# Kernel optimization log

Measured on AMD Instinct MI355X. Metric: run time of the kernel, lower is better.

## Reference

```python
import jax, jax.numpy as jnp
import numpy as np

DEPTH = 10
LAMDA = 1e-3
EPS = 1e-7


def setup_inputs() -> dict:
    key = jax.random.key(0)
    k1, k2, k3, k4 = jax.random.split(key, 4)
    B, D, O = 16384, 512, 256
    N = 2 ** DEPTH - 1        # inner nodes
    L = 2 ** DEPTH            # leaves
    data = jax.random.normal(k1, (B, D), jnp.float32)
    # small scale on W keeps sigmoid away from saturation (like nn.Linear init)
    W = jax.random.normal(k2, (N, D + 1), jnp.float32) * 0.02
    beta = jax.random.normal(k3, (N,), jnp.float32)
    param = jax.random.normal(k4, (L, O), jnp.float32)
    return {"data": data, "W": W, "beta": beta, "param": param}


def reference(data, W, beta, param):
    B = data.shape[0]
    L = param.shape[0]
    # _data_augment_: prepend constant 1 as bias feature -> [B, D+1]
    x = jnp.concatenate([jnp.ones((B, 1), data.dtype), data], axis=1)
    # inner_nodes: sigmoid(beta * linear(x)) -> [B, N]
    p = jax.nn.sigmoid(beta * (x @ W.T))
    # per-node (go-left, go-right) probabilities -> [B, N, 2]
    path_prob = jnp.stack([p, 1.0 - p], axis=2)

    mu = jnp.ones((B, 1), data.dtype)          # path prob of root
    penalty = jnp.asarray(0.0, data.dtype)
    begin = 0
    for layer in range(DEPTH):                  # fixed small loop over depth
        n = 2 ** layer
        pp = path_prob[:, begin:begin + n, :].reshape(B, 2 * n)  # [B, 2n]
        mu_rep = jnp.repeat(mu, 2, axis=1)                        # [B, 2n]
        # vectorized form of the per-node penalty loop
        alpha = jnp.sum(pp * mu_rep, axis=0) / (jnp.sum(mu_rep, axis=0) + EPS)
        alpha = jnp.clip(alpha, EPS, 1.0 - EPS)
        coeff = LAMDA * (2.0 ** (-layer))
        penalty = penalty - coeff * 0.5 * jnp.sum(jnp.log(alpha) + jnp.log(1.0 - alpha))
        mu = mu_rep * pp
        begin += n

    # mu: [B, leaf_num]; leaf_nodes: mu @ softmax(param)
    dist = jax.nn.softmax(param, axis=1)       # [L, O]
    output = mu @ dist                          # [B, O]
    # greatest_path_probability: hard argmax leaf (one-hot @ dist == gather)
    ids = jnp.argmax(mu, axis=1)
    prediction = dist[ids]                      # [B, O]
    # LogProb=True
    return (jnp.log(prediction), jnp.log(output), penalty, W)
```

## Files before the change

### kernel.cpp

```cpp
#include <hip/hip_runtime.h>
#include <hip/hip_bf16.h>

#define B_ROWS 16384
#define DDIM   512
#define NNODES 1023
#define NLEAF  1024
#define ODIM   256
#define LAMDA  1e-3
#define EPSV   1e-7f

typedef __bf16 bf16x8v __attribute__((ext_vector_type(8)));
typedef _Float16 f16x8 __attribute__((ext_vector_type(8)));
typedef float  f32x16v __attribute__((ext_vector_type(16)));

__device__ __forceinline__ float bf2f(unsigned short u) {
    return __uint_as_float(((unsigned)u) << 16);
}

__device__ __forceinline__ void gload16h(const _Float16* g, _Float16* l) {
    __builtin_amdgcn_global_load_lds(
        (const __attribute__((address_space(1))) unsigned int*)g,
        (__attribute__((address_space(3))) unsigned int*)l, 16, 0, 0);
}
__device__ __forceinline__ void gload16b(const __hip_bfloat16* g, __hip_bfloat16* l) {
    __builtin_amdgcn_global_load_lds(
        (const __attribute__((address_space(1))) unsigned int*)g,
        (__attribute__((address_space(3))) unsigned int*)l, 16, 0, 0);
}

__global__ __launch_bounds__(256)
void prep_all(const float* __restrict__ data, const float* __restrict__ W,
              const float* __restrict__ param,
              _Float16* __restrict__ Dh, _Float16* __restrict__ Dl,
              _Float16* __restrict__ Wh, _Float16* __restrict__ Wl,
              float* __restrict__ outW,
              float* __restrict__ logdist, __hip_bfloat16* __restrict__ DT2)
{
    __shared__ float red[4], red2[4];
    if (blockIdx.x < 4096) {
        int idx = blockIdx.x * 256 + threadIdx.x;
        int b  = idx >> 6;
        int k8 = idx & 63;
        const float4 v0 = *reinterpret_cast<const float4*>(&data[(size_t)b * DDIM + k8 * 8]);
        const float4 v1 = *reinterpret_cast<const float4*>(&data[(size_t)b * DDIM + k8 * 8 + 4]);
        float a[8] = {v0.x, v0.y, v0.z, v0.w, v1.x, v1.y, v1.z, v1.w};
        __align__(16) _Float16 h[8], l[8];
#pragma unroll
        for (int j = 0; j < 8; ++j) {
            h[j] = (_Float16)a[j];
            l[j] = (_Float16)((a[j] - (float)h[j]) * 2048.f);
        }
        int by = b >> 8, tl = (b >> 5) & 7, ln = (b & 31) | ((k8 & 1) << 5), ks = k8 >> 1;
        size_t off = ((((size_t)by * 32 + ks) * 8 + tl) * 64 + ln) * 8;
        *reinterpret_cast<ulonglong2*>(&Dh[off]) = *reinterpret_cast<const ulonglong2*>(h);
        *reinterpret_cast<ulonglong2*>(&Dl[off]) = *reinterpret_cast<const ulonglong2*>(l);
    } else if (blockIdx.x < 4352) {
        int idx = (blockIdx.x - 4096) * 256 + threadIdx.x;
        int t  = idx & 255;
        int ks = (idx >> 8) & 31;
        int nb = idx >> 13;
        int tm = t >> 6, ln = t & 63;
        int node = nb * 128 + tm * 32 + (ln & 31);
        int k = ks * 16 + (ln >> 5) * 8;
        __align__(16) _Float16 h[8], l[8];
        if (node < NNODES) {
#pragma unroll
            for (int j = 0; j < 8; ++j) {
                float a = W[(size_t)node * 513 + 1 + k + j];
                h[j] = (_Float16)a;
                l[j] = (_Float16)((a - (float)h[j]) * 2048.f);
            }
        } else {
#pragma unroll
            for (int j = 0; j < 8; ++j) { h[j] = (_Float16)0.f; l[j] = (_Float16)0.f; }
        }
        size_t off = (size_t)idx * 8;
        *reinterpret_cast<ulonglong2*>(&Wh[off]) = *reinterpret_cast<const ulonglong2*>(h);
        *reinterpret_cast<ulonglong2*>(&Wl[off]) = *reinterpret_cast<const ulonglong2*>(l);
    } else if (blockIdx.x < 6404) {
        int i = (blockIdx.x - 4352) * 256 + threadIdx.x;
        if (i < NNODES * 513) outW[i] = W[i];
    } else {
        int l = blockIdx.x - 6404;
        int o = threadIdx.x;
        float x = param[(size_t)l * ODIM + o];
        float m = x;
#pragma unroll
        for (int s = 1; s < 64; s <<= 1) m = fmaxf(m, __shfl_xor(m, s, 64));
        if ((o & 63) == 0) red[o >> 6] = m;
        __syncthreads();
        m = fmaxf(fmaxf(red[0], red[1]), fmaxf(red[2], red[3]));
        float e = expf(x - m);
        float s = e;
#pragma unroll
        for (int k = 1; k < 64; k <<= 1) s += __shfl_xor(s, k, 64);
        if ((o & 63) == 0) red2[o >> 6] = s;
        __syncthreads();
        s = red2[0] + red2[1] + red2[2] + red2[3];
        float d = e / s;
        logdist[(size_t)l * ODIM + o] = logf(d);
        int kc = l >> 4, kk = l & 15;
        int lane = (o & 31) | ((kk >> 3) << 5);
        DT2[(((size_t)kc * 8 + (o >> 5)) * 64 + lane) * 8 + (kk & 7)] = __float2bfloat16(d);
    }
}

__global__ __launch_bounds__(512, 2)
void gemm1_mfma(const _Float16* __restrict__ Wh, const _Float16* __restrict__ Wl,
                const _Float16* __restrict__ Dh, const _Float16* __restrict__ Dl,
                const float* __restrict__ W, const float* __restrict__ beta,
                float* __restrict__ PT)
{
    __shared__ _Float16 lds[3][24576];
    const int tid = threadIdx.x;
    const int lane = tid & 63;
    const int wv = tid >> 6;
    const int wm = wv & 1, wn = wv >> 1;
    const int id = blockIdx.x;
    const int xcd = id & 7, slot = id >> 3;
    const int bx = slot & 7;
    const int by = xcd * 8 + (slot >> 3);
    const size_t wofs = (size_t)bx * 65536 + tid * 8;
    const size_t dofs = (size_t)by * 131072 + tid * 8;

    f32x16v acc_h[2][2] = {};
    f32x16v acc_l[2][2] = {};

#define STAGE(buf, tt) do { \
        const size_t wo = wofs + (size_t)(tt) * 4096; \
        const size_t dd = dofs + (size_t)(tt) * 8192; \
        gload16h(Wh + wo,        &lds[buf][tid * 8]); \
        gload16h(Wl + wo,        &lds[buf][4096  + tid * 8]); \
        gload16h(Dh + dd,        &lds[buf][8192  + tid * 8]); \
        gload16h(Dh + dd + 4096, &lds[buf][12288 + tid * 8]); \
        gload16h(Dl + dd,        &lds[buf][16384 + tid * 8]); \
        gload16h(Dl + dd + 4096, &lds[buf][20480 + tid * 8]); \
    } while (0)

#define LOADFRAG(L, kcl) do { \
        _Pragma("unroll") \
        for (int i = 0; i < 2; ++i) { \
            int ao = (((kcl) * 4 + wm * 2 + i) * 64 + lane) * 8; \
            ah[i] = *reinterpret_cast<const f16x8*>(&(L)[ao]); \
            al[i] = *reinterpret_cast<const f16x8*>(&(L)[4096 + ao]); \
        } \
        _Pragma("unroll") \
        for (int j = 0; j < 2; ++j) { \
            int bo = (((kcl) * 8 + wn * 2 + j) * 64 + lane) * 8; \
            bh[j] = *reinterpret_cast<const f16x8*>(&(L)[8192 + bo]); \
            bl[j] = *reinterpret_cast<const f16x8*>(&(L)[16384 + bo]); \
        } \
    } while (0)

#define MFMA12() do { \
        _Pragma("unroll") \
        for (int i = 0; i < 2; ++i) \
        _Pragma("unroll") \
        for (int j = 0; j < 2; ++j) { \
            acc_h[i][j] = __builtin_amdgcn_mfma_f32_32x32x16_f16(ah[i], bh[j], acc_h[i][j], 0, 0, 0); \
            acc_l[i][j] = __builtin_amdgcn_mfma_f32_32x32x16_f16(ah[i], bl[j], acc_l[i][j], 0, 0, 0); \
            acc_l[i][j] = __builtin_amdgcn_mfma_f32_32x32x16_f16(al[i], bh[j], acc_l[i][j], 0, 0, 0); \
        } \
    } while (0)

    STAGE(0, 0);
    STAGE(1, 1);
    asm volatile("s_waitcnt vmcnt(6)" ::: "memory");
    __builtin_amdgcn_s_barrier();

    for (int t = 0; t < 16; ++t) {
        const _Float16* L = lds[t % 3];
        f16x8 ah[2], al[2], bh[2], bl[2];

        LOADFRAG(L, 0);
        if (t + 2 < 16) STAGE((t + 2) % 3, t + 2);
        __builtin_amdgcn_s_barrier();
        asm volatile("s_waitcnt lgkmcnt(0)" ::: "memory");
        __builtin_amdgcn_s_setprio(1);
        MFMA12();
        __builtin_amdgcn_s_setprio(0);
        __builtin_amdgcn_s_barrier();

        LOADFRAG(L, 1);
        __builtin_amdgcn_s_barrier();
        asm volatile("s_waitcnt lgkmcnt(0)" ::: "memory");
        __builtin_amdgcn_s_setprio(1);
        MFMA12();
        __builtin_amdgcn_s_setprio(0);
        if (t < 14) asm volatile("s_waitcnt vmcnt(6)" ::: "memory");
        else        asm volatile("s_waitcnt vmcnt(0)" ::: "memory");
        __builtin_amdgcn_s_barrier();
    }
#undef STAGE
#undef LOADFRAG
#undef MFMA12

#pragma unroll
    for (int i = 0; i < 2; ++i) {
#pragma unroll
        for (int r = 0; r < 16; ++r) {
            int node = bx * 128 + wm * 64 + i * 32 + ((r & 3) + 8 * (r >> 2) + 4 * (lane >> 5));
            if (node < NNODES) {
                float w0 = W[(size_t)node * 513];
                float bt = beta[node];
#pragma unroll
                for (int j = 0; j < 2; ++j) {
                    float z = acc_h[i][j][r] + acc_l[i][j][r] * 4.8828125e-4f;
                    float s = bt * (z + w0);
                    float p = 1.f / (1.f + expf(-s));
                    PT[(size_t)node * B_ROWS + by * 256 + wn * 64 + j * 32 + (lane & 31)] = p;
                }
            }
        }
    }
}

__global__ __launch_bounds__(256, 4)
void tree_pass(const float* __restrict__ PT,
               __hip_bfloat16* __restrict__ MU2,
               float* __restrict__ pval,
               int*   __restrict__ pidx)
{
    const int tid = threadIdx.x;
    const int rb = blockIdx.x & 63;
    const int g  = blockIdx.x >> 6;
    const int b  = rb * 256 + tid;

    const int c4 = 15 + g;
    const int n3 = (c4 - 1) >> 1;
    const int n2 = (n3 - 1) >> 1;
    const int n1 = (n2 - 1) >> 1;
    const float pc4 = PT[(size_t)c4 * B_ROWS + b];
    const float pn3 = PT[(size_t)n3 * B_ROWS + b];
    const float pn2 = PT[(size_t)n2 * B_ROWS + b];
    const float pn1 = PT[(size_t)n1 * B_ROWS + b];
    const float pn0 = PT[b];
    float pre = ((c4 & 1) ? pn3 : 1.f - pn3)
              * ((n3 & 1) ? pn2 : 1.f - pn2)
              * ((n2 & 1) ? pn1 : 1.f - pn1)
              * ((n1 & 1) ? pn0 : 1.f - pn0);
    float root[2] = { pre * pc4, pre * (1.f - pc4) };

    __align__(16) __hip_bfloat16 mbv[64];
    float bestv = -1.f; int besti = 0;
#pragma unroll
    for (int ss = 0; ss < 2; ++ss) {
        const int t = 2 * g + ss;
        float s[32];
#pragma unroll
        for (int u = 1; u < 32; ++u) {
            int lvl = 31 - __clz(u);
            int node = ((32 << lvl) - 1) + t * (1 << lvl) + (u - (1 << lvl));
            s[u] = PT[(size_t)node * B_ROWS + b];
        }
        float w[64];
        w[1] = root[ss];
#pragma unroll
        for (int u = 1; u < 32; ++u) {
            w[2 * u]     = w[u] * s[u];
            w[2 * u + 1] = w[u] * (1.f - s[u]);
        }
#pragma unroll
        for (int q = 0; q < 32; ++q) {
            float lv = w[32 + q];
            mbv[ss * 32 + q] = __float2bfloat16(lv);
            if (lv > bestv) { bestv = lv; besti = t * 32 + q; }
        }
    }
    {
        const int mb_ = b >> 7, mt_ = (b >> 5) & 3, lnlo = b & 31;
        const ulonglong2* src = reinterpret_cast<const ulonglong2*>(mbv);
#pragma unroll
        for (int c = 0; c < 4; ++c) {
            size_t base16 = (((size_t)mb_ * 64 + g * 4 + c) * 4 + mt_) * 64;
            *reinterpret_cast<ulonglong2*>(&MU2[(base16 + lnlo) * 8])      = src[c * 2];
            *reinterpret_cast<ulonglong2*>(&MU2[(base16 + 32 + lnlo) * 8]) = src[c * 2 + 1];
        }
    }
    pval[(size_t)g * B_ROWS + b] = bestv;
    pidx[(size_t)g * B_ROWS + b] = besti;
}

__global__ __launch_bounds__(256)
void colsum_argmax(const __hip_bfloat16* __restrict__ MU2, float* __restrict__ partial,
                   const float* __restrict__ pval, const int* __restrict__ pidx,
                   const float* __restrict__ logdist, float* __restrict__ out0)
{
    __shared__ float red[4][2][8];
    __shared__ int sid[64];
    const int t = threadIdx.x;
    if (blockIdx.x < 256) {
        const int blk = blockIdx.x;
        const int kc = blk >> 2, mbg = blk & 3;
        const int w = t >> 6, ln = t & 63;
        float a[8] = {0.f, 0.f, 0.f, 0.f, 0.f, 0.f, 0.f, 0.f};
        for (int it = 0; it < 32; ++it) {
            int it2 = it * 4 + w;
            int mb = mbg * 32 + (it2 >> 2), mt = it2 & 3;
            size_t a16 = (((size_t)mb * 64 + kc) * 4 + mt) * 64 + ln;
            ulonglong2 u = *reinterpret_cast<const ulonglong2*>(&MU2[a16 * 8]);
            const unsigned short* hs = reinterpret_cast<const unsigned short*>(&u);
#pragma unroll
            for (int j = 0; j < 8; ++j) a[j] += bf2f(hs[j]);
        }
#pragma unroll
        for (int m = 1; m < 32; m <<= 1)
#pragma unroll
            for (int j = 0; j < 8; ++j) a[j] += __shfl_xor(a[j], m, 64);
        if ((ln & 31) == 0) {
#pragma unroll
            for (int j = 0; j < 8; ++j) red[w][ln >> 5][j] = a[j];
        }
        __syncthreads();
        if (t < 16) {
            float s = red[0][t >> 3][t & 7] + red[1][t >> 3][t & 7]
                    + red[2][t >> 3][t & 7] + red[3][t >> 3][t & 7];
            partial[(size_t)mbg * NLEAF + kc * 16 + t] = s;
        }
    } else {
        const int blk = blockIdx.x - 256;
        if (t < 64) {
            int row = blk * 64 + t;
            float bv = -1.f; int bi = 0;
            for (int g = 0; g < 16; ++g) {
                float v = pval[(size_t)g * B_ROWS + row];
                if (v > bv) { bv = v; bi = pidx[(size_t)g * B_ROWS + row]; }
            }
            sid[t] = bi;
        }
        __syncthreads();
        for (int rr = 0; rr < 64; ++rr) {
            int id = sid[rr];
            out0[(size_t)(blk * 64 + rr) * ODIM + t] = logdist[(size_t)id * ODIM + t];
        }
    }
}

__global__ __launch_bounds__(256)
void gemm2_penalty(const __hip_bfloat16* __restrict__ MU2,
                   const __hip_bfloat16* __restrict__ DT2,
                   float* __restrict__ out1,
                   const float* __restrict__ partial, float* __restrict__ out_pen)
{
    __shared__ __hip_bfloat16 ldsA[2][2048];
    __shared__ __hip_bfloat16 ldsB[2][8192];
    __shared__ float M[2048];
    __shared__ double dred[256];
    const int tid = threadIdx.x;
    if (blockIdx.x == 256) {
        for (int i = tid; i < 1024; i += 256)
            M[1024 + i] = partial[i] + partial[NLEAF + i] + partial[2 * NLEAF + i] + partial[3 * NLEAF + i];
        __syncthreads();
        for (int n = 512; n >= 1; n >>= 1) {
            for (int u = n + tid; u < 2 * n; u += 256) M[u] = M[2 * u] + M[2 * u + 1];
            __syncthreads();
        }
        double acc = 0.0;
        for (int u = 2 + tid; u < 2048; u += 256) {
            int lvl = 31 - __clz(u);
            float a = M[u] / (M[u >> 1] + EPSV);
            a = fminf(fmaxf(a, EPSV), 1.f - EPSV);
            float term = logf(a) + logf(1.f - a);
            acc -= ldexp((double)LAMDA * 0.5, 1 - lvl) * (double)term;
        }
        dred[tid] = acc;
        __syncthreads();
        for (int s = 128; s > 0; s >>= 1) {
            if (tid < s) dred[tid] += dred[tid + s];
            __syncthreads();
        }
        if (tid == 0) out_pen[0] = (float)dred[0];
        return;
    }
    const int lane = tid & 63;
    const int w = tid >> 6;
    const int blk = blockIdx.x;
    const int m0 = blk * 64;
    const int mb = blk >> 1;
    const int mtbase = (blk & 1) * 2;
    const int s_kcl = tid >> 7, s_mti = (tid >> 6) & 1, s_ln = tid & 63;

    f32x16v acc[2][2] = {};

#define STAGE2(buf, kc0) do { \
        size_t sa16 = (((size_t)mb * 64 + (kc0) + s_kcl) * 4 + mtbase + s_mti) * 64 + s_ln; \
        gload16b(MU2 + sa16 * 8, &ldsA[buf][tid * 8]); \
        gload16b(DT2 + ((size_t)(kc0) * 512 + tid) * 8,             &ldsB[buf][tid * 8]); \
        gload16b(DT2 + ((size_t)(kc0) * 512 + 256 + tid) * 8,       &ldsB[buf][2048 + tid * 8]); \
        gload16b(DT2 + ((size_t)((kc0) + 1) * 512 + tid) * 8,       &ldsB[buf][4096 + tid * 8]); \
        gload16b(DT2 + ((size_t)((kc0) + 1) * 512 + 256 + tid) * 8, &ldsB[buf][6144 + tid * 8]); \
    } while (0)

    STAGE2(0, 0);
    for (int it = 0; it < 32; ++it) {
        const int cur = it & 1;
        if (it + 1 < 32) {
            STAGE2(cur ^ 1, 2 * (it + 1));
            asm volatile("s_waitcnt vmcnt(5)" ::: "memory");
        } else {
            asm volatile("s_waitcnt vmcnt(0)" ::: "memory");
        }
        __builtin_amdgcn_s_barrier();
        bf16x8v a[2][2], bb[2][2];
#pragma unroll
        for (int kcl = 0; kcl < 2; ++kcl)
#pragma unroll
            for (int i = 0; i < 2; ++i) {
                a[kcl][i]  = *reinterpret_cast<const bf16x8v*>(&ldsA[cur][((kcl * 2 + i) * 64 + lane) * 8]);
                bb[kcl][i] = *reinterpret_cast<const bf16x8v*>(&ldsB[cur][((kcl * 8 + 2 * w + i) * 64 + lane) * 8]);
            }
        __builtin_amdgcn_s_setprio(1);
#pragma unroll
        for (int kcl = 0; kcl < 2; ++kcl)
#pragma unroll
            for (int i = 0; i < 2; ++i)
#pragma unroll
                for (int j = 0; j < 2; ++j)
                    acc[i][j] = __builtin_amdgcn_mfma_f32_32x32x16_bf16(a[kcl][i], bb[kcl][j], acc[i][j], 0, 0, 0);
        __builtin_amdgcn_s_setprio(0);
        asm volatile("s_waitcnt lgkmcnt(0)" ::: "memory");
        __builtin_amdgcn_s_barrier();
    }
#undef STAGE2
#pragma unroll
    for (int i = 0; i < 2; ++i)
#pragma unroll
        for (int j = 0; j < 2; ++j)
#pragma unroll
            for (int r = 0; r < 16; ++r) {
                int row = m0 + i * 32 + (r & 3) + 8 * (r >> 2) + 4 * (lane >> 5);
                int col = w * 64 + j * 32 + (lane & 31);
                out1[(size_t)row * ODIM + col] = logf(acc[i][j][r]);
            }
}

extern "C" void kernel_launch(void* const* d_in, const int* in_sizes, int n_in,
                              void* d_out, int out_size, void* d_ws, size_t ws_size,
                              hipStream_t stream)
{
    (void)in_sizes; (void)n_in; (void)out_size; (void)ws_size;
    const float* data  = (const float*)d_in[0];
    const float* W     = (const float*)d_in[1];
    const float* beta  = (const float*)d_in[2];
    const float* param = (const float*)d_in[3];
    float* out = (float*)d_out;

    char* ws = (char*)d_ws;
    size_t off = 0;
    float* PT = (float*)(ws + off);                   off += (size_t)NNODES * B_ROWS * 4;
    char* X = ws + off;                               off += 2 * 1048576 + 2 * 16777216;
    _Float16* Wh = (_Float16*)(X);
    _Float16* Wl = (_Float16*)(X + 1048576);
    _Float16* Dh = (_Float16*)(X + 2 * 1048576);
    _Float16* Dl = (_Float16*)(X + 2 * 1048576 + 16777216);
    __hip_bfloat16* MU2 = (__hip_bfloat16*)(X + 2 * 1048576);
    __hip_bfloat16* DT2 = (__hip_bfloat16*)(ws + off); off += (size_t)ODIM * NLEAF * 2;
    float* logdist = (float*)(ws + off);              off += (size_t)NLEAF * ODIM * 4;
    float* partial = (float*)(ws + off);              off += (size_t)4 * NLEAF * 4;
    float* pval    = (float*)(ws + off);              off += (size_t)16 * B_ROWS * 4;
    int*   pidx    = (int*)(ws + off);                off += (size_t)16 * B_ROWS * 4;

    float* out_logpred = out;
    float* out_logout  = out + (size_t)B_ROWS * ODIM;
    float* out_pen     = out + 2 * (size_t)B_ROWS * ODIM;
    float* out_W       = out_pen + 1;

    prep_all<<<7428, 256, 0, stream>>>(data, W, param, Dh, Dl, Wh, Wl, out_W, logdist, DT2);

    gemm1_mfma<<<512, 512, 0, stream>>>(Wh, Wl, Dh, Dl, W, beta, PT);

    tree_pass<<<1024, 256, 0, stream>>>(PT, MU2, pval, pidx);

    colsum_argmax<<<512, 256, 0, stream>>>(MU2, partial, pval, pidx, logdist, out_logpred);

    gemm2_penalty<<<257, 256, 0, stream>>>(MU2, DT2, out_logout, partial, out_pen);
}
```

Before: 151.3 us.

## Shrink gemm1 tile to 128x128 with double buffering for higher occupancy

The first GEMM now uses 128x128 output tiles instead of 128x256, doubling the grid to 1024 blocks. The LDS ring drops from three large stages to two small ones over a finer K loop, and the launch bounds are raised to allow four blocks per CU. The goal is more concurrent waves to hide load latency and better CU fill. The cost is less operand reuse per block, twice as many barriers, and more redundant global/L2 traffic for the W tiles.

```diff
diff --git a/kernel.cpp b/kernel.cpp
--- a/kernel.cpp
+++ b/kernel.cpp
@@ -105,13 +105,13 @@
     }
 }
 
-__global__ __launch_bounds__(512, 2)
+__global__ __launch_bounds__(512, 4)
 void gemm1_mfma(const _Float16* __restrict__ Wh, const _Float16* __restrict__ Wl,
                 const _Float16* __restrict__ Dh, const _Float16* __restrict__ Dl,
                 const float* __restrict__ W, const float* __restrict__ beta,
                 float* __restrict__ PT)
 {
-    __shared__ _Float16 lds[3][24576];
+    __shared__ _Float16 lds[2][8192];
     const int tid = threadIdx.x;
     const int lane = tid & 63;
     const int wv = tid >> 6;
@@ -119,81 +119,60 @@
     const int id = blockIdx.x;
     const int xcd = id & 7, slot = id >> 3;
     const int bx = slot & 7;
-    const int by = xcd * 8 + (slot >> 3);
-    const size_t wofs = (size_t)bx * 65536 + tid * 8;
-    const size_t dofs = (size_t)by * 131072 + tid * 8;
-
-    f32x16v acc_h[2][2] = {};
-    f32x16v acc_l[2][2] = {};
-
-#define STAGE(buf, tt) do { \
-        const size_t wo = wofs + (size_t)(tt) * 4096; \
-        const size_t dd = dofs + (size_t)(tt) * 8192; \
-        gload16h(Wh + wo,        &lds[buf][tid * 8]); \
-        gload16h(Wl + wo,        &lds[buf][4096  + tid * 8]); \
-        gload16h(Dh + dd,        &lds[buf][8192  + tid * 8]); \
-        gload16h(Dh + dd + 4096, &lds[buf][12288 + tid * 8]); \
-        gload16h(Dl + dd,        &lds[buf][16384 + tid * 8]); \
-        gload16h(Dl + dd + 4096, &lds[buf][20480 + tid * 8]); \
+    const int by = xcd * 16 + (slot >> 3);
+    const int by256 = by >> 1;
+    const int tlb = (by & 1) * 4;
+
+    const int q  = tid & 255;
+    const int qt = q >> 6, qn = q & 63;
+    const _Float16* Wsel = (tid < 256) ? Wh : Wl;
+    const _Float16* Dsel = (tid < 256) ? Dh : Dl;
+    const _Float16* wsrc = Wsel + (size_t)bx * 65536 + qt * 512 + qn * 8;
+    const _Float16* dsrc = Dsel + (size_t)by256 * 131072 + (tlb + qt) * 512 + qn * 8;
+
+    f32x16v acc_h[2] = {};
+    f32x16v acc_l[2] = {};
+
+#define STAGE(buf, ks) do { \
+        gload16h(wsrc + (size_t)(ks) * 2048, &lds[buf][tid * 8]); \
+        gload16h(dsrc + (size_t)(ks) * 4096, &lds[buf][4096 + tid * 8]); \
     } while (0)
 
-#define LOADFRAG(L, kcl) do { \
-        _Pragma("unroll") \
-        for (int i = 0; i < 2; ++i) { \
-            int ao = (((kcl) * 4 + wm * 2 + i) * 64 + lane) * 8; \
-            ah[i] = *reinterpret_cast<const f16x8*>(&(L)[ao]); \
-            al[i] = *reinterpret_cast<const f16x8*>(&(L)[4096 + ao]); \
-        } \
-        _Pragma("unroll") \
-        for (int j = 0; j < 2; ++j) { \
-            int bo = (((kcl) * 8 + wn * 2 + j) * 64 + lane) * 8; \
-            bh[j] = *reinterpret_cast<const f16x8*>(&(L)[8192 + bo]); \
-            bl[j] = *reinterpret_cast<const f16x8*>(&(L)[16384 + bo]); \
-        } \
-    } while (0)
-
-#define MFMA12() do { \
-        _Pragma("unroll") \
-        for (int i = 0; i < 2; ++i) \
-        _Pragma("unroll") \
-        for (int j = 0; j < 2; ++j) { \
-            acc_h[i][j] = __builtin_amdgcn_mfma_f32_32x32x16_f16(ah[i], bh[j], acc_h[i][j], 0, 0, 0); \
-            acc_l[i][j] = __builtin_amdgcn_mfma_f32_32x32x16_f16(ah[i], bl[j], acc_l[i][j], 0, 0, 0); \
-            acc_l[i][j] = __builtin_amdgcn_mfma_f32_32x32x16_f16(al[i], bh[j], acc_l[i][j], 0, 0, 0); \
-        } \
-    } while (0)
-
     STAGE(0, 0);
-    STAGE(1, 1);
-    asm volatile("s_waitcnt vmcnt(6)" ::: "memory");
-    __builtin_amdgcn_s_barrier();
-
-    for (int t = 0; t < 16; ++t) {
-        const _Float16* L = lds[t % 3];
-        f16x8 ah[2], al[2], bh[2], bl[2];
-
-        LOADFRAG(L, 0);
-        if (t + 2 < 16) STAGE((t + 2) % 3, t + 2);
+    for (int t = 0; t < 32; ++t) {
+        const int cur = t & 1;
+        if (t < 31) {
+            STAGE(cur ^ 1, t + 1);
+            asm volatile("s_waitcnt vmcnt(2)" ::: "memory");
+        } else {
+            asm volatile("s_waitcnt vmcnt(0)" ::: "memory");
+        }
         __builtin_amdgcn_s_barrier();
+
+        f16x8 ah[2], al[2], bh, bl;
+#pragma unroll
+        for (int i = 0; i < 2; ++i) {
+            int ao = ((wm * 2 + i) * 64 + lane) * 8;
+            ah[i] = *reinterpret_cast<const f16x8*>(&lds[cur][ao]);
+            al[i] = *reinterpret_cast<const f16x8*>(&lds[cur][2048 + ao]);
+        }
+        {
+            int bo = (wn * 64 + lane) * 8;
+            bh = *reinterpret_cast<const f16x8*>(&lds[cur][4096 + bo]);
+            bl = *reinterpret_cast<const f16x8*>(&lds[cur][6144 + bo]);
+        }
+        __builtin_amdgcn_s_setprio(1);
+#pragma unroll
+        for (int i = 0; i < 2; ++i) {
+            acc_h[i] = __builtin_amdgcn_mfma_f32_32x32x16_f16(ah[i], bh, acc_h[i], 0, 0, 0);
+            acc_l[i] = __builtin_amdgcn_mfma_f32_32x32x16_f16(ah[i], bl, acc_l[i], 0, 0, 0);
+            acc_l[i] = __builtin_amdgcn_mfma_f32_32x32x16_f16(al[i], bh, acc_l[i], 0, 0, 0);
+        }
+        __builtin_amdgcn_s_setprio(0);
         asm volatile("s_waitcnt lgkmcnt(0)" ::: "memory");
-        __builtin_amdgcn_s_setprio(1);
-        MFMA12();
-        __builtin_amdgcn_s_setprio(0);
         __builtin_amdgcn_s_barrier();
-
-        LOADFRAG(L, 1);
-        __builtin_amdgcn_s_barrier();
-        asm volatile("s_waitcnt lgkmcnt(0)" ::: "memory");
-        __builtin_amdgcn_s_setprio(1);
-        MFMA12();
-        __builtin_amdgcn_s_setprio(0);
-        if (t < 14) asm volatile("s_waitcnt vmcnt(6)" ::: "memory");
-        else        asm volatile("s_waitcnt vmcnt(0)" ::: "memory");
-        __builtin_amdgcn_s_barrier();
     }
 #undef STAGE
-#undef LOADFRAG
-#undef MFMA12
 
 #pragma unroll
     for (int i = 0; i < 2; ++i) {
@@ -203,13 +182,10 @@
             if (node < NNODES) {
                 float w0 = W[(size_t)node * 513];
                 float bt = beta[node];
-#pragma unroll
-                for (int j = 0; j < 2; ++j) {
-                    float z = acc_h[i][j][r] + acc_l[i][j][r] * 4.8828125e-4f;
-                    float s = bt * (z + w0);
-                    float p = 1.f / (1.f + expf(-s));
-                    PT[(size_t)node * B_ROWS + by * 256 + wn * 64 + j * 32 + (lane & 31)] = p;
-                }
+                float z = acc_h[i][r] + acc_l[i][r] * 4.8828125e-4f;
+                float s = bt * (z + w0);
+                float p = 1.f / (1.f + expf(-s));
+                PT[(size_t)node * B_ROWS + by * 128 + wn * 32 + (lane & 31)] = p;
             }
         }
     }
@@ -467,7 +443,7 @@
 
     prep_all<<<7428, 256, 0, stream>>>(data, W, param, Dh, Dl, Wh, Wl, out_W, logdist, DT2);
 
-    gemm1_mfma<<<512, 512, 0, stream>>>(Wh, Wl, Dh, Dl, W, beta, PT);
+    gemm1_mfma<<<1024, 512, 0, stream>>>(Wh, Wl, Dh, Dl, W, beta, PT);
 
     tree_pass<<<1024, 256, 0, stream>>>(PT, MU2, pval, pidx);
 
```

Result: no change. 151.0 us (-0.2%).
